# Optimization experiments

Measured on AMD Instinct MI355X. Metric: run time of the kernel, lower is better.

Reference implementation:

```python
import jax, jax.numpy as jnp
import numpy as np

B, I, O, H = 32768, 16, 16, 512  # batch, in_dim, out_dim, hid_dim
NEG_SLOPE = 0.2


def setup_inputs() -> dict:
    key = jax.random.key(0)
    k_x, k_w1, k_b1, k_w2, k_b2 = jax.random.split(key, 5)
    x = jax.random.normal(k_x, (B, I), dtype=jnp.float32)

    # Per-output first-layer weights, init like the torch module:
    # randn, small |w|<0.01 replaced by +-0.01, then masked by jacobian_support row.
    support = jnp.ones((O, I), dtype=jnp.float32)  # jacobian_support (all ones)
    W1 = jax.random.normal(k_w1, (O, H, I), dtype=jnp.float32)
    adjusted = 0.02 * (W1 >= 0).astype(jnp.float32) - 0.01
    W1 = jnp.where(jnp.abs(W1) < 0.01, adjusted, W1) * support[:, None, :]

    # Biases / second layer: torch default Linear init, uniform(-1/sqrt(fan_in), 1/sqrt(fan_in))
    bnd1 = 1.0 / np.sqrt(I)
    bnd2 = 1.0 / np.sqrt(H)
    b1 = jax.random.uniform(k_b1, (O, H), dtype=jnp.float32, minval=-bnd1, maxval=bnd1)
    W2 = jax.random.uniform(k_w2, (O, H), dtype=jnp.float32, minval=-bnd2, maxval=bnd2)
    b2 = jax.random.uniform(k_b2, (O,), dtype=jnp.float32, minval=-bnd2, maxval=bnd2)
    return {"x": x, "W1": W1, "b1": b1, "W2": W2, "b2": b2}


def reference(x, W1, b1, W2, b2):
    # Fused batched GEMM over all out_dim heads (replaces the python loop).
    # hidden: [B, O, H]
    h = jnp.einsum('bi,ohi->boh', x, W1) + b1
    h = jnp.where(h >= 0, h, NEG_SLOPE * h)  # LeakyReLU(0.2)
    # second layer maps H -> 1 per head; concatenated output: [B, O]
    out = jnp.einsum('boh,oh->bo', h, W2) + b2
    return out
```

## Files before the change

kernel.cpp:

```cpp
#include <hip/hip_runtime.h>


#define B_DIM 32768
#define I_DIM 16
#define O_DIM 16
#define H_DIM 512

typedef _Float16 f16x4 __attribute__((ext_vector_type(4)));
typedef _Float16 f16x8 __attribute__((ext_vector_type(8)));
typedef __fp16   h16x2 __attribute__((ext_vector_type(2)));
typedef float    f32x4 __attribute__((ext_vector_type(4)));
typedef int      i32x2 __attribute__((ext_vector_type(2)));
typedef int      i32x4 __attribute__((ext_vector_type(4)));

#define A1P_OFF  0
#define W2F_OFF  (256 * 1024)
#define VL_OFF   (512 * 1024)
#define C0_OFF   (521 * 1024)

__global__ void prep_all(const float* __restrict__ W1, const float* __restrict__ b1,
                         const float* __restrict__ W2, const float* __restrict__ b2,
                         ushort* __restrict__ a1p, ushort* __restrict__ w2f,
                         ushort* __restrict__ vl, float* __restrict__ c0b2) {
    int blk = blockIdx.x;
    if (blk < 64) {
        int t = blk * 256 + threadIdx.x;
        int l = t & 63, p = (t >> 6) & 15, o = t >> 10;
        int row = l & 15, kg = l >> 4;
        f16x8 v;
#pragma unroll
        for (int j = 0; j < 4; ++j)
            v[j] = (_Float16)W1[(size_t)(o * H_DIM + (2 * p) * 16 + row) * I_DIM + kg * 4 + j];
#pragma unroll
        for (int j = 0; j < 4; ++j)
            v[4 + j] = (_Float16)W1[(size_t)(o * H_DIM + (2 * p + 1) * 16 + row) * I_DIM + kg * 4 + j];
        *reinterpret_cast<f16x8*>(a1p + (size_t)t * 8) = v;
    } else if (blk < 128) {
        int t = (blk - 64) * 256 + threadIdx.x;
        int l = t & 63, p = (t >> 6) & 15, o = t >> 10;
        int kg = l >> 4;
        f16x8 v;
#pragma unroll
        for (int j = 0; j < 8; ++j) {
            int h = p * 32 + ((j >> 2) & 1) * 16 + kg * 4 + (j & 3);
            v[j] = (_Float16)(0.4f * W2[o * H_DIM + h]);
        }
        *reinterpret_cast<f16x8*>(w2f + (size_t)t * 8) = v;
    } else {
        __shared__ float red[256];
        __shared__ float v_sm[16];
        const int o = blk - 128, t = threadIdx.x;
        const int i = t & 15, hc = t >> 4;
        float acc = 0.f;
        for (int hh = 0; hh < 32; ++hh) {
            int h = hc * 32 + hh;
            acc = fmaf(W2[o * H_DIM + h], W1[(size_t)(o * H_DIM + h) * I_DIM + i], acc);
        }
        red[t] = acc;
        __syncthreads();
        if (t < 16) {
            float s = 0.f;
#pragma unroll
            for (int k = 0; k < 16; ++k) s += red[t + 16 * k];
            v_sm[t] = 0.6f * s;
        }
        float cacc = 0.f;
        for (int h = t; h < H_DIM; h += 256) cacc += W2[o * H_DIM + h] * b1[o * H_DIM + h];
        __syncthreads();
        red[t] = cacc;
        __syncthreads();
        if (t == 0) {
            float s = 0.f;
            for (int k = 0; k < 256; ++k) s += red[k];
            c0b2[o] = 0.6f * s + b2[o];
        }
        if (t < 64) {
            int kg = t >> 4;
            f16x4 v;
#pragma unroll
            for (int j = 0; j < 4; ++j) v[j] = (_Float16)v_sm[kg * 4 + j];
            *reinterpret_cast<f16x4*>(vl + (size_t)(o * 64 + t) * 4) = v;
        }
    }
}

__global__ __launch_bounds__(256, 4) void mlp_main(
    const float* __restrict__ x, const ushort* __restrict__ a1p_u,
    const ushort* __restrict__ w2f_u, const ushort* __restrict__ vl_u,
    const float* __restrict__ c0b2, const float* __restrict__ b1,
    float* __restrict__ out) {
    __shared__ f16x8 sm_a1[1024];
    __shared__ f16x8 sm_w2[1024];
    __shared__ float sm_b1[512];
    __shared__ f16x4 sm_vl[64];

    const int tid = threadIdx.x;
    const int o   = blockIdx.x & 15;
    const int grp = blockIdx.x >> 4;

    const f16x8* ga = reinterpret_cast<const f16x8*>(a1p_u) + (size_t)o * 1024;
    const f16x8* gw = reinterpret_cast<const f16x8*>(w2f_u) + (size_t)o * 1024;
#pragma unroll
    for (int i = 0; i < 4; ++i) sm_a1[i * 256 + tid] = ga[i * 256 + tid];
#pragma unroll
    for (int i = 0; i < 4; ++i) sm_w2[i * 256 + tid] = gw[i * 256 + tid];
    sm_b1[tid]       = b1[o * H_DIM + tid];
    sm_b1[tid + 256] = b1[o * H_DIM + tid + 256];
    if (tid < 64) sm_vl[tid] = reinterpret_cast<const f16x4*>(vl_u)[o * 64 + tid];
    __syncthreads();

    const int lane = tid & 63, w = tid >> 6;
    const int col = lane & 15, kg = lane >> 4;
    const int tile0 = grp * 32 + w * 8;

    f16x4 xf[8];
#pragma unroll
    for (int t = 0; t < 8; ++t) {
        const f32x4 xr = *reinterpret_cast<const f32x4*>(
            x + (size_t)((tile0 + t) * 16 + col) * I_DIM + kg * 4);
        h16x2 q0 = __builtin_amdgcn_cvt_pkrtz(xr[0], xr[1]);
        h16x2 q1 = __builtin_amdgcn_cvt_pkrtz(xr[2], xr[3]);
        i32x2 xi; xi[0] = __builtin_bit_cast(int, q0); xi[1] = __builtin_bit_cast(int, q1);
        xf[t] = __builtin_bit_cast(f16x4, xi);
    }

    const float c0 = c0b2[o];
    const f32x4 linC = {c0, c0, c0, c0};
    const f16x4 vlf = sm_vl[lane];
    f32x4 acc[8];
#pragma unroll
    for (int t = 0; t < 8; ++t)
        acc[t] = __builtin_amdgcn_mfma_f32_16x16x16f16(xf[t], vlf, linC, 0, 0, 0);

#pragma unroll 2
    for (int p = 0; p < 16; ++p) {
        const f16x8 a1pair = sm_a1[p * 64 + lane];
        const f16x4 A1a = __builtin_shufflevector(a1pair, a1pair, 0, 1, 2, 3);
        const f16x4 A1b = __builtin_shufflevector(a1pair, a1pair, 4, 5, 6, 7);
        const f16x8 W2f = sm_w2[p * 64 + lane];
        const f32x4 bC0 = *reinterpret_cast<const f32x4*>(&sm_b1[p * 32 + kg * 4]);
        const f32x4 bC1 = *reinterpret_cast<const f32x4*>(&sm_b1[p * 32 + 16 + kg * 4]);
#pragma unroll
        for (int t = 0; t < 8; ++t) {
            f32x4 d0 = __builtin_amdgcn_mfma_f32_16x16x16f16(A1a, xf[t], bC0, 0, 0, 0);
            f32x4 d1 = __builtin_amdgcn_mfma_f32_16x16x16f16(A1b, xf[t], bC1, 0, 0, 0);
            h16x2 p0 = __builtin_amdgcn_cvt_pkrtz(fabsf(d0[0]), fabsf(d0[1]));
            h16x2 p1 = __builtin_amdgcn_cvt_pkrtz(fabsf(d0[2]), fabsf(d0[3]));
            h16x2 p2 = __builtin_amdgcn_cvt_pkrtz(fabsf(d1[0]), fabsf(d1[1]));
            h16x2 p3 = __builtin_amdgcn_cvt_pkrtz(fabsf(d1[2]), fabsf(d1[3]));
            i32x4 ai;
            ai[0] = __builtin_bit_cast(int, p0); ai[1] = __builtin_bit_cast(int, p1);
            ai[2] = __builtin_bit_cast(int, p2); ai[3] = __builtin_bit_cast(int, p3);
            f16x8 A2 = __builtin_bit_cast(f16x8, ai);
            acc[t] = __builtin_amdgcn_mfma_f32_16x16x32_f16(A2, W2f, acc[t], 0, 0, 0);
        }
    }

    if (col < 4) {
#pragma unroll
        for (int t = 0; t < 8; ++t) {
            float v = (col == 0) ? acc[t][0] : (col == 1) ? acc[t][1]
                    : (col == 2) ? acc[t][2] : acc[t][3];
            out[(size_t)((tile0 + t) * 16 + kg * 4 + col) * O_DIM + o] = v;
        }
    }
}

extern "C" void kernel_launch(void* const* d_in, const int* in_sizes, int n_in,
                              void* d_out, int out_size, void* d_ws, size_t ws_size,
                              hipStream_t stream) {
    const float* x  = (const float*)d_in[0];
    const float* W1 = (const float*)d_in[1];
    const float* b1 = (const float*)d_in[2];
    const float* W2 = (const float*)d_in[3];
    const float* b2 = (const float*)d_in[4];
    float* out = (float*)d_out;
    char* ws = (char*)d_ws;

    ushort* a1p  = (ushort*)(ws + A1P_OFF);
    ushort* w2f  = (ushort*)(ws + W2F_OFF);
    ushort* vl   = (ushort*)(ws + VL_OFF);
    float*  c0b2 = (float*)(ws + C0_OFF);

    prep_all<<<144, 256, 0, stream>>>(W1, b1, W2, b2, a1p, w2f, vl, c0b2);
    mlp_main<<<1024, 256, 0, stream>>>(x, a1p, w2f, vl, c0b2, b1, out);
}
```

Measured before the change: 31.55 us.

## Split hidden dimension across waves with register-resident weights and LDS reduction

Each wave now holds a fixed quarter of the hidden dimension's W1, W2 and b1 fragments in registers and loops over all 32 batch tiles of the block. Previously each wave took 8 batch tiles and streamed every weight fragment from shared memory. The four per-wave partial sums are combined through a small double-buffered LDS array with a barrier per tile. This drops the bulk weight staging into LDS and the per-iteration LDS reads, but adds 32 block-wide barriers and serial x loads inside the loop.

Result: slower. 35.88 us (+13.7%).

```diff
diff --git a/kernel.cpp b/kernel.cpp
--- a/kernel.cpp
+++ b/kernel.cpp
@@ -13,30 +13,27 @@
 typedef int      i32x2 __attribute__((ext_vector_type(2)));
 typedef int      i32x4 __attribute__((ext_vector_type(4)));
 
-#define A1P_OFF  0
+#define A1F_OFF  0
 #define W2F_OFF  (256 * 1024)
 #define VL_OFF   (512 * 1024)
 #define C0_OFF   (521 * 1024)
 
 __global__ void prep_all(const float* __restrict__ W1, const float* __restrict__ b1,
                          const float* __restrict__ W2, const float* __restrict__ b2,
-                         ushort* __restrict__ a1p, ushort* __restrict__ w2f,
+                         ushort* __restrict__ a1f, ushort* __restrict__ w2f,
                          ushort* __restrict__ vl, float* __restrict__ c0b2) {
     int blk = blockIdx.x;
-    if (blk < 64) {
+    if (blk < 128) {
         int t = blk * 256 + threadIdx.x;
-        int l = t & 63, p = (t >> 6) & 15, o = t >> 10;
+        int l = t & 63, ct = (t >> 6) & 31, o = t >> 11;
         int row = l & 15, kg = l >> 4;
-        f16x8 v;
+        f16x4 v;
 #pragma unroll
         for (int j = 0; j < 4; ++j)
-            v[j] = (_Float16)W1[(size_t)(o * H_DIM + (2 * p) * 16 + row) * I_DIM + kg * 4 + j];
-#pragma unroll
-        for (int j = 0; j < 4; ++j)
-            v[4 + j] = (_Float16)W1[(size_t)(o * H_DIM + (2 * p + 1) * 16 + row) * I_DIM + kg * 4 + j];
-        *reinterpret_cast<f16x8*>(a1p + (size_t)t * 8) = v;
-    } else if (blk < 128) {
-        int t = (blk - 64) * 256 + threadIdx.x;
+            v[j] = (_Float16)W1[(size_t)(o * H_DIM + ct * 16 + row) * I_DIM + kg * 4 + j];
+        *reinterpret_cast<f16x4*>(a1f + (size_t)t * 4) = v;
+    } else if (blk < 192) {
+        int t = (blk - 128) * 256 + threadIdx.x;
         int l = t & 63, p = (t >> 6) & 15, o = t >> 10;
         int kg = l >> 4;
         f16x8 v;
@@ -49,7 +46,7 @@
     } else {
         __shared__ float red[256];
         __shared__ float v_sm[16];
-        const int o = blk - 128, t = threadIdx.x;
+        const int o = blk - 192, t = threadIdx.x;
         const int i = t & 15, hc = t >> 4;
         float acc = 0.f;
         for (int hh = 0; hh < 32; ++hh) {
@@ -85,65 +82,54 @@
 }
 
 __global__ __launch_bounds__(256, 4) void mlp_main(
-    const float* __restrict__ x, const ushort* __restrict__ a1p_u,
+    const float* __restrict__ x, const ushort* __restrict__ a1f_u,
     const ushort* __restrict__ w2f_u, const ushort* __restrict__ vl_u,
     const float* __restrict__ c0b2, const float* __restrict__ b1,
     float* __restrict__ out) {
-    __shared__ f16x8 sm_a1[1024];
-    __shared__ f16x8 sm_w2[1024];
-    __shared__ float sm_b1[512];
-    __shared__ f16x4 sm_vl[64];
+    __shared__ float smred[2][64];
 
     const int tid = threadIdx.x;
     const int o   = blockIdx.x & 15;
     const int grp = blockIdx.x >> 4;
-
-    const f16x8* ga = reinterpret_cast<const f16x8*>(a1p_u) + (size_t)o * 1024;
-    const f16x8* gw = reinterpret_cast<const f16x8*>(w2f_u) + (size_t)o * 1024;
-#pragma unroll
-    for (int i = 0; i < 4; ++i) sm_a1[i * 256 + tid] = ga[i * 256 + tid];
-#pragma unroll
-    for (int i = 0; i < 4; ++i) sm_w2[i * 256 + tid] = gw[i * 256 + tid];
-    sm_b1[tid]       = b1[o * H_DIM + tid];
-    sm_b1[tid + 256] = b1[o * H_DIM + tid + 256];
-    if (tid < 64) sm_vl[tid] = reinterpret_cast<const f16x4*>(vl_u)[o * 64 + tid];
-    __syncthreads();
-
     const int lane = tid & 63, w = tid >> 6;
     const int col = lane & 15, kg = lane >> 4;
-    const int tile0 = grp * 32 + w * 8;
 
-    f16x4 xf[8];
+    const f16x4* ga = reinterpret_cast<const f16x4*>(a1f_u)
+                    + ((size_t)(o * 32 + w * 8) * 64 + lane);
+    f16x4 A1r[8];
 #pragma unroll
-    for (int t = 0; t < 8; ++t) {
+    for (int c = 0; c < 8; ++c) A1r[c] = ga[c * 64];
+    const f16x8* gw = reinterpret_cast<const f16x8*>(w2f_u)
+                    + ((size_t)(o * 16 + w * 4) * 64 + lane);
+    f16x8 W2r[4];
+#pragma unroll
+    for (int q = 0; q < 4; ++q) W2r[q] = gw[q * 64];
+    f32x4 b1r[8];
+#pragma unroll
+    for (int c = 0; c < 8; ++c)
+        b1r[c] = *reinterpret_cast<const f32x4*>(b1 + o * H_DIM + (w * 8 + c) * 16 + kg * 4);
+    const f16x4 vlf = reinterpret_cast<const f16x4*>(vl_u)[o * 64 + lane];
+    const float c0 = c0b2[o];
+    const f32x4 linC = {c0, c0, c0, c0};
+    const f32x4 zero = {0.f, 0.f, 0.f, 0.f};
+
+    for (int j = 0; j < 32; ++j) {
+        const int tile = grp * 32 + j;
         const f32x4 xr = *reinterpret_cast<const f32x4*>(
-            x + (size_t)((tile0 + t) * 16 + col) * I_DIM + kg * 4);
+            x + (size_t)(tile * 16 + col) * I_DIM + kg * 4);
         h16x2 q0 = __builtin_amdgcn_cvt_pkrtz(xr[0], xr[1]);
         h16x2 q1 = __builtin_amdgcn_cvt_pkrtz(xr[2], xr[3]);
         i32x2 xi; xi[0] = __builtin_bit_cast(int, q0); xi[1] = __builtin_bit_cast(int, q1);
-        xf[t] = __builtin_bit_cast(f16x4, xi);
-    }
+        const f16x4 xf = __builtin_bit_cast(f16x4, xi);
 
-    const float c0 = c0b2[o];
-    const f32x4 linC = {c0, c0, c0, c0};
-    const f16x4 vlf = sm_vl[lane];
-    f32x4 acc[8];
+        f32x4 acc;
+        if (w == 0) acc = __builtin_amdgcn_mfma_f32_16x16x16f16(xf, vlf, linC, 0, 0, 0);
+        else        acc = zero;
+
 #pragma unroll
-    for (int t = 0; t < 8; ++t)
-        acc[t] = __builtin_amdgcn_mfma_f32_16x16x16f16(xf[t], vlf, linC, 0, 0, 0);
-
-#pragma unroll 2
-    for (int p = 0; p < 16; ++p) {
-        const f16x8 a1pair = sm_a1[p * 64 + lane];
-        const f16x4 A1a = __builtin_shufflevector(a1pair, a1pair, 0, 1, 2, 3);
-        const f16x4 A1b = __builtin_shufflevector(a1pair, a1pair, 4, 5, 6, 7);
-        const f16x8 W2f = sm_w2[p * 64 + lane];
-        const f32x4 bC0 = *reinterpret_cast<const f32x4*>(&sm_b1[p * 32 + kg * 4]);
-        const f32x4 bC1 = *reinterpret_cast<const f32x4*>(&sm_b1[p * 32 + 16 + kg * 4]);
-#pragma unroll
-        for (int t = 0; t < 8; ++t) {
-            f32x4 d0 = __builtin_amdgcn_mfma_f32_16x16x16f16(A1a, xf[t], bC0, 0, 0, 0);
-            f32x4 d1 = __builtin_amdgcn_mfma_f32_16x16x16f16(A1b, xf[t], bC1, 0, 0, 0);
+        for (int q = 0; q < 4; ++q) {
+            f32x4 d0 = __builtin_amdgcn_mfma_f32_16x16x16f16(A1r[2 * q],     xf, b1r[2 * q],     0, 0, 0);
+            f32x4 d1 = __builtin_amdgcn_mfma_f32_16x16x16f16(A1r[2 * q + 1], xf, b1r[2 * q + 1], 0, 0, 0);
             h16x2 p0 = __builtin_amdgcn_cvt_pkrtz(fabsf(d0[0]), fabsf(d0[1]));
             h16x2 p1 = __builtin_amdgcn_cvt_pkrtz(fabsf(d0[2]), fabsf(d0[3]));
             h16x2 p2 = __builtin_amdgcn_cvt_pkrtz(fabsf(d1[0]), fabsf(d1[1]));
@@ -152,16 +138,19 @@
             ai[0] = __builtin_bit_cast(int, p0); ai[1] = __builtin_bit_cast(int, p1);
             ai[2] = __builtin_bit_cast(int, p2); ai[3] = __builtin_bit_cast(int, p3);
             f16x8 A2 = __builtin_bit_cast(f16x8, ai);
-            acc[t] = __builtin_amdgcn_mfma_f32_16x16x32_f16(A2, W2f, acc[t], 0, 0, 0);
+            acc = __builtin_amdgcn_mfma_f32_16x16x32_f16(A2, W2r[q], acc, 0, 0, 0);
         }
-    }
 
-    if (col < 4) {
-#pragma unroll
-        for (int t = 0; t < 8; ++t) {
-            float v = (col == 0) ? acc[t][0] : (col == 1) ? acc[t][1]
-                    : (col == 2) ? acc[t][2] : acc[t][3];
-            out[(size_t)((tile0 + t) * 16 + kg * 4 + col) * O_DIM + o] = v;
+        if (col < 4) {
+            float v = (col == 0) ? acc[0] : (col == 1) ? acc[1]
+                    : (col == 2) ? acc[2] : acc[3];
+            smred[j & 1][w * 16 + kg * 4 + col] = v;
+        }
+        __syncthreads();
+        if (tid < 16) {
+            const float* r = smred[j & 1];
+            out[(size_t)(tile * 16 + tid) * O_DIM + o] =
+                r[tid] + r[16 + tid] + r[32 + tid] + r[48 + tid];
         }
     }
 }
@@ -177,11 +166,11 @@
     float* out = (float*)d_out;
     char* ws = (char*)d_ws;
 
-    ushort* a1p  = (ushort*)(ws + A1P_OFF);
+    ushort* a1f  = (ushort*)(ws + A1F_OFF);
     ushort* w2f  = (ushort*)(ws + W2F_OFF);
     ushort* vl   = (ushort*)(ws + VL_OFF);
     float*  c0b2 = (float*)(ws + C0_OFF);
 
-    prep_all<<<144, 256, 0, stream>>>(W1, b1, W2, b2, a1p, w2f, vl, c0b2);
-    mlp_main<<<1024, 256, 0, stream>>>(x, a1p, w2f, vl, c0b2, b1, out);
+    prep_all<<<208, 256, 0, stream>>>(W1, b1, W2, b2, a1f, w2f, vl, c0b2);
+    mlp_main<<<1024, 256, 0, stream>>>(x, a1f, w2f, vl, c0b2, b1, out);
 }
```

## Fuse weight prep into main kernel and double block size to 512 threads

Applied to the files above, without the earlier changes.

Drops the separate prep kernel. Each block of the main kernel now converts its head's W1/W2 to fp16 MFMA layout in shared memory and computes the linear-term vector and constant itself. The block size rises from 256 to 512 threads and the grid halves to 512 blocks, so each block covers 64 tiles and the redundant per-block prep is spread over more work. This removes a kernel launch and a workspace round trip, at the cost of repeating the weight conversion and reductions in every block and a heavier prologue before the MFMA loop.

Result: faster. 27.75 us (-12.0%).

```diff
diff --git a/kernel.cpp b/kernel.cpp
--- a/kernel.cpp
+++ b/kernel.cpp
@@ -13,105 +13,83 @@
 typedef int      i32x2 __attribute__((ext_vector_type(2)));
 typedef int      i32x4 __attribute__((ext_vector_type(4)));
 
-#define A1P_OFF  0
-#define W2F_OFF  (256 * 1024)
-#define VL_OFF   (512 * 1024)
-#define C0_OFF   (521 * 1024)
-
-__global__ void prep_all(const float* __restrict__ W1, const float* __restrict__ b1,
-                         const float* __restrict__ W2, const float* __restrict__ b2,
-                         ushort* __restrict__ a1p, ushort* __restrict__ w2f,
-                         ushort* __restrict__ vl, float* __restrict__ c0b2) {
-    int blk = blockIdx.x;
-    if (blk < 64) {
-        int t = blk * 256 + threadIdx.x;
-        int l = t & 63, p = (t >> 6) & 15, o = t >> 10;
-        int row = l & 15, kg = l >> 4;
-        f16x8 v;
-#pragma unroll
-        for (int j = 0; j < 4; ++j)
-            v[j] = (_Float16)W1[(size_t)(o * H_DIM + (2 * p) * 16 + row) * I_DIM + kg * 4 + j];
-#pragma unroll
-        for (int j = 0; j < 4; ++j)
-            v[4 + j] = (_Float16)W1[(size_t)(o * H_DIM + (2 * p + 1) * 16 + row) * I_DIM + kg * 4 + j];
-        *reinterpret_cast<f16x8*>(a1p + (size_t)t * 8) = v;
-    } else if (blk < 128) {
-        int t = (blk - 64) * 256 + threadIdx.x;
-        int l = t & 63, p = (t >> 6) & 15, o = t >> 10;
-        int kg = l >> 4;
-        f16x8 v;
-#pragma unroll
-        for (int j = 0; j < 8; ++j) {
-            int h = p * 32 + ((j >> 2) & 1) * 16 + kg * 4 + (j & 3);
-            v[j] = (_Float16)(0.4f * W2[o * H_DIM + h]);
-        }
-        *reinterpret_cast<f16x8*>(w2f + (size_t)t * 8) = v;
-    } else {
-        __shared__ float red[256];
-        __shared__ float v_sm[16];
-        const int o = blk - 128, t = threadIdx.x;
-        const int i = t & 15, hc = t >> 4;
-        float acc = 0.f;
-        for (int hh = 0; hh < 32; ++hh) {
-            int h = hc * 32 + hh;
-            acc = fmaf(W2[o * H_DIM + h], W1[(size_t)(o * H_DIM + h) * I_DIM + i], acc);
-        }
-        red[t] = acc;
-        __syncthreads();
-        if (t < 16) {
-            float s = 0.f;
-#pragma unroll
-            for (int k = 0; k < 16; ++k) s += red[t + 16 * k];
-            v_sm[t] = 0.6f * s;
-        }
-        float cacc = 0.f;
-        for (int h = t; h < H_DIM; h += 256) cacc += W2[o * H_DIM + h] * b1[o * H_DIM + h];
-        __syncthreads();
-        red[t] = cacc;
-        __syncthreads();
-        if (t == 0) {
-            float s = 0.f;
-            for (int k = 0; k < 256; ++k) s += red[k];
-            c0b2[o] = 0.6f * s + b2[o];
-        }
-        if (t < 64) {
-            int kg = t >> 4;
-            f16x4 v;
-#pragma unroll
-            for (int j = 0; j < 4; ++j) v[j] = (_Float16)v_sm[kg * 4 + j];
-            *reinterpret_cast<f16x4*>(vl + (size_t)(o * 64 + t) * 4) = v;
-        }
-    }
-}
-
-__global__ __launch_bounds__(256, 4) void mlp_main(
-    const float* __restrict__ x, const ushort* __restrict__ a1p_u,
-    const ushort* __restrict__ w2f_u, const ushort* __restrict__ vl_u,
-    const float* __restrict__ c0b2, const float* __restrict__ b1,
-    float* __restrict__ out) {
+__global__ __launch_bounds__(512, 4) void mlp_fused(
+    const float* __restrict__ x, const float* __restrict__ W1,
+    const float* __restrict__ b1, const float* __restrict__ W2,
+    const float* __restrict__ b2, float* __restrict__ out) {
     __shared__ f16x8 sm_a1[1024];
     __shared__ f16x8 sm_w2[1024];
     __shared__ float sm_b1[512];
-    __shared__ f16x4 sm_vl[64];
+    __shared__ float red[512];
+    __shared__ float v_sm[16];
+    __shared__ float c_sm;
 
     const int tid = threadIdx.x;
     const int o   = blockIdx.x & 15;
     const int grp = blockIdx.x >> 4;
+    const float* W1o = W1 + (size_t)o * H_DIM * I_DIM;
+    const float* W2o = W2 + (size_t)o * H_DIM;
+    const float* b1o = b1 + (size_t)o * H_DIM;
 
-    const f16x8* ga = reinterpret_cast<const f16x8*>(a1p_u) + (size_t)o * 1024;
-    const f16x8* gw = reinterpret_cast<const f16x8*>(w2f_u) + (size_t)o * 1024;
 #pragma unroll
-    for (int i = 0; i < 4; ++i) sm_a1[i * 256 + tid] = ga[i * 256 + tid];
+    for (int i = 0; i < 2; ++i) {
+        const int e = tid + 512 * i;
+        const int l = e & 63, p = e >> 6;
+        const int row = l & 15, kg = l >> 4;
+        const float* a_base = W1o + ((size_t)(2 * p * 16 + row) * I_DIM + kg * 4);
+        const f32x4 a0 = *reinterpret_cast<const f32x4*>(a_base);
+        const f32x4 a1v = *reinterpret_cast<const f32x4*>(a_base + 16 * I_DIM);
+        f16x8 va;
 #pragma unroll
-    for (int i = 0; i < 4; ++i) sm_w2[i * 256 + tid] = gw[i * 256 + tid];
-    sm_b1[tid]       = b1[o * H_DIM + tid];
-    sm_b1[tid + 256] = b1[o * H_DIM + tid + 256];
-    if (tid < 64) sm_vl[tid] = reinterpret_cast<const f16x4*>(vl_u)[o * 64 + tid];
+        for (int j = 0; j < 4; ++j) { va[j] = (_Float16)a0[j]; va[4 + j] = (_Float16)a1v[j]; }
+        sm_a1[e] = va;
+        const float* w_base = W2o + p * 32 + kg * 4;
+        const f32x4 w0 = *reinterpret_cast<const f32x4*>(w_base);
+        const f32x4 w1v = *reinterpret_cast<const f32x4*>(w_base + 16);
+        f16x8 vw;
+#pragma unroll
+        for (int j = 0; j < 4; ++j) {
+            vw[j]     = (_Float16)(0.4f * w0[j]);
+            vw[4 + j] = (_Float16)(0.4f * w1v[j]);
+        }
+        sm_w2[e] = vw;
+    }
+    sm_b1[tid] = b1o[tid];
+
+    {
+        const int i = tid & 15, hc = tid >> 4;
+        float acc = 0.f;
+#pragma unroll
+        for (int hh = 0; hh < 16; ++hh) {
+            const int h = hc * 16 + hh;
+            acc = fmaf(W2o[h], W1o[(size_t)h * I_DIM + i], acc);
+        }
+        red[tid] = acc;
+    }
+    __syncthreads();
+    if (tid < 16) {
+        float s = 0.f;
+#pragma unroll
+        for (int k = 0; k < 32; ++k) s += red[tid + 16 * k];
+        v_sm[tid] = 0.6f * s;
+    }
+    float cpart = W2o[tid] * b1o[tid];
+    __syncthreads();
+    red[tid] = cpart;
+    __syncthreads();
+    if (tid < 64) {
+        float s = 0.f;
+#pragma unroll
+        for (int k = 0; k < 8; ++k) s += red[tid + 64 * k];
+#pragma unroll
+        for (int m = 1; m <= 32; m <<= 1) s += __shfl_xor(s, m, 64);
+        if (tid == 0) c_sm = 0.6f * s + b2[o];
+    }
     __syncthreads();
 
     const int lane = tid & 63, w = tid >> 6;
     const int col = lane & 15, kg = lane >> 4;
-    const int tile0 = grp * 32 + w * 8;
+    const int tile0 = grp * 64 + w * 8;
 
     f16x4 xf[8];
 #pragma unroll
@@ -124,9 +102,12 @@
         xf[t] = __builtin_bit_cast(f16x4, xi);
     }
 
-    const float c0 = c0b2[o];
+    f16x4 vlf;
+#pragma unroll
+    for (int j = 0; j < 4; ++j) vlf[j] = (_Float16)v_sm[kg * 4 + j];
+    const float c0 = c_sm;
     const f32x4 linC = {c0, c0, c0, c0};
-    const f16x4 vlf = sm_vl[lane];
+
     f32x4 acc[8];
 #pragma unroll
     for (int t = 0; t < 8; ++t)
@@ -175,13 +156,6 @@
     const float* W2 = (const float*)d_in[3];
     const float* b2 = (const float*)d_in[4];
     float* out = (float*)d_out;
-    char* ws = (char*)d_ws;
 
-    ushort* a1p  = (ushort*)(ws + A1P_OFF);
-    ushort* w2f  = (ushort*)(ws + W2F_OFF);
-    ushort* vl   = (ushort*)(ws + VL_OFF);
-    float*  c0b2 = (float*)(ws + C0_OFF);
-
-    prep_all<<<144, 256, 0, stream>>>(W1, b1, W2, b2, a1p, w2f, vl, c0b2);
-    mlp_main<<<1024, 256, 0, stream>>>(x, a1p, w2f, vl, c0b2, b1, out);
+    mlp_fused<<<512, 512, 0, stream>>>(x, W1, b1, W2, b2, out);
 }
```
